# Kernel tuning notes

Hardware: AMD Instinct MI355X
Metric: run time of the kernel (lower is better)

Reference implementation:

```python
import jax, jax.numpy as jnp
import numpy as np

V, P, TY, D, H, L, B, T = 30522, 512, 2, 768, 12, 12, 8, 512
DF = 4 * D


def layer_norm(x, g, b, eps=1e-5):
    m = jnp.mean(x, axis=-1, keepdims=True)
    v = jnp.var(x, axis=-1, keepdims=True)
    return (x - m) * jax.lax.rsqrt(v + eps) * g + b


def new_gelu(x):
    c = np.sqrt(2.0 / np.pi).astype(np.float32)
    return 0.5 * x * (1.0 + jnp.tanh(c * (x + 0.044715 * x * x * x)))


def setup_inputs() -> dict:
    key = jax.random.key(0)
    ks = jax.random.split(key, 10)
    s = 0.02
    n = lambda k, shape: (jax.random.normal(k, shape, jnp.float32) * s)
    return dict(
        input_ids=jax.random.randint(ks[0], (B, T), 0, V),
        token_type_ids=jax.random.randint(ks[1], (B, T), 0, TY),
        attention_mask=jnp.ones((B, T), jnp.float32),
        word_emb=n(ks[2], (V, D)),
        pos_emb=n(ks[3], (P, D)),
        type_emb=n(ks[4], (TY, D)),
        emb_ln_g=jnp.ones((D,), jnp.float32), emb_ln_b=jnp.zeros((D,), jnp.float32),
        ln1_g=jnp.ones((L, D), jnp.float32), ln1_b=jnp.zeros((L, D), jnp.float32),
        wqkv=n(ks[5], (L, D, 3 * D)), bqkv=jnp.zeros((L, 3 * D), jnp.float32),
        wproj=n(ks[6], (L, D, D)) / np.sqrt(2 * L).astype(np.float32),
        bproj=jnp.zeros((L, D), jnp.float32),
        ln2_g=jnp.ones((L, D), jnp.float32), ln2_b=jnp.zeros((L, D), jnp.float32),
        wfc=n(ks[7], (L, D, DF)), bfc=jnp.zeros((L, DF), jnp.float32),
        wfc2=n(ks[8], (L, DF, D)) / np.sqrt(2 * L).astype(np.float32),
        bfc2=jnp.zeros((L, D), jnp.float32),
    )


def reference(input_ids, token_type_ids, attention_mask, word_emb, pos_emb, type_emb,
              emb_ln_g, emb_ln_b, ln1_g, ln1_b, wqkv, bqkv, wproj, bproj,
              ln2_g, ln2_b, wfc, bfc, wfc2, bfc2):
    Bx, Tx = input_ids.shape
    hd = D // H
    scale = np.float32(1.0 / np.sqrt(hd))
    # embeddings: word + position + token-type, then LayerNorm (dropout = 0)
    x = word_emb[input_ids] + pos_emb[:Tx][None, :, :] + type_emb[token_type_ids]
    x = layer_norm(x, emb_ln_g, emb_ln_b)
    # additive mask bias, broadcast over heads and query positions: [B,1,1,T]
    mask_bias = (1.0 - attention_mask)[:, None, None, :] * (-10000.0)

    def block(x, p):
        l1g, l1b, wq, bq, wp, bp, l2g, l2b, wf, bf, w2, b2 = p
        h = layer_norm(x, l1g, l1b)
        qkv = h @ wq + bq                                   # [B,T,3D]
        q, k, v = jnp.split(qkv, 3, axis=-1)
        q = q.reshape(Bx, Tx, H, hd).transpose(0, 2, 1, 3)  # [B,H,T,hd]
        k = k.reshape(Bx, Tx, H, hd).transpose(0, 2, 1, 3)
        v = v.reshape(Bx, Tx, H, hd).transpose(0, 2, 1, 3)
        att = jnp.einsum('bhqd,bhkd->bhqk', q, k) * scale + mask_bias
        att = jax.nn.softmax(att, axis=-1)
        y = jnp.einsum('bhqk,bhkd->bhqd', att, v)
        y = y.transpose(0, 2, 1, 3).reshape(Bx, Tx, D)
        x = x + (y @ wp + bp)                               # attn residual
        h2 = layer_norm(x, l2g, l2b)
        h2 = new_gelu(h2 @ wf + bf) @ w2 + b2               # GELU MLP
        return x + h2, None

    x, _ = jax.lax.scan(block, x, (ln1_g, ln1_b, wqkv, bqkv, wproj, bproj,
                                   ln2_g, ln2_b, wfc, bfc, wfc2, bfc2))
    # baseline MLM head: weight tied to word embeddings, no bias
    logits = x @ word_emb.T                                 # [B,T,V]
    return logits
```

## Files before the change

### kernel.cpp

```cpp
#include <hip/hip_runtime.h>
#include <hip/hip_bf16.h>

typedef unsigned short u16;
typedef __attribute__((ext_vector_type(4))) float f32x4;
typedef __attribute__((ext_vector_type(8))) __bf16 bf16x8;

#define DEV static __device__ __forceinline__

DEV float b2f(u16 v) { return __uint_as_float(((unsigned)v) << 16); }

DEV u16 f2b(float f) {
  unsigned u = __float_as_uint(f);
  return (u16)((u + 0x7fffu + ((u >> 16) & 1u)) >> 16);
}

DEV unsigned pk2(float a, float b) {
  return (unsigned)f2b(a) | ((unsigned)f2b(b) << 16);
}

DEV void gload16(const void* g, void* l) {
  __builtin_amdgcn_global_load_lds(
      (__attribute__((address_space(1))) void*)g,
      (__attribute__((address_space(3))) void*)l, 16, 0, 0);
}

DEV float wave_sum(float v) {
  #pragma unroll
  for (int o = 32; o; o >>= 1) v += __shfl_xor(v, o, 64);
  return v;
}

__global__ __launch_bounds__(256)
void embed_ln_k(const int* __restrict__ ids, const int* __restrict__ tts,
                const float* __restrict__ we, const float* __restrict__ pe,
                const float* __restrict__ te, const float* __restrict__ g,
                const float* __restrict__ bb, float* __restrict__ x) {
  const int t = blockIdx.x;
  const int pos = t & 511;
  const int tid = threadIdx.x, lane = tid & 63, w = tid >> 6;
  const int id = ids[t], tt = tts[t];
  __shared__ float red[8];
  float e[3];
  #pragma unroll
  for (int k = 0; k < 3; k++) {
    int d = tid + k * 256;
    e[k] = we[(size_t)id * 768 + d] + pe[(size_t)pos * 768 + d] + te[(size_t)tt * 768 + d];
  }
  float s = wave_sum(e[0] + e[1] + e[2]);
  if (lane == 0) red[w] = s;
  __syncthreads();
  const float mean = (red[0] + red[1] + red[2] + red[3]) * (1.f / 768.f);
  float v2 = 0.f;
  #pragma unroll
  for (int k = 0; k < 3; k++) { float d = e[k] - mean; v2 += d * d; }
  v2 = wave_sum(v2);
  if (lane == 0) red[4 + w] = v2;
  __syncthreads();
  const float var = (red[4] + red[5] + red[6] + red[7]) * (1.f / 768.f);
  const float rstd = rsqrtf(var + 1e-5f);
  #pragma unroll
  for (int k = 0; k < 3; k++) {
    int d = tid + k * 256;
    x[(size_t)t * 768 + d] = (e[k] - mean) * rstd * g[d] + bb[d];
  }
}

__global__ __launch_bounds__(256)
void ln_k(const float* __restrict__ xin, const float* __restrict__ g,
          const float* __restrict__ bb, u16* __restrict__ out) {
  const int lane = threadIdx.x & 63, w = threadIdx.x >> 6;
  const int t = blockIdx.x * 4 + w;
  const float4* x4 = (const float4*)(xin + (size_t)t * 768);
  float4 e[3];
  #pragma unroll
  for (int k = 0; k < 3; k++) e[k] = x4[k * 64 + lane];
  float s = 0.f;
  #pragma unroll
  for (int k = 0; k < 3; k++) s += e[k].x + e[k].y + e[k].z + e[k].w;
  s = wave_sum(s);
  const float mean = s * (1.f / 768.f);
  float v2 = 0.f;
  #pragma unroll
  for (int k = 0; k < 3; k++) {
    float a = e[k].x - mean, b = e[k].y - mean, c = e[k].z - mean, d = e[k].w - mean;
    v2 += a * a + b * b + c * c + d * d;
  }
  v2 = wave_sum(v2);
  const float rstd = rsqrtf(v2 * (1.f / 768.f) + 1e-5f);
  uint2* o2 = (uint2*)(out + (size_t)t * 768);
  #pragma unroll
  for (int k = 0; k < 3; k++) {
    float4 gv = ((const float4*)g)[k * 64 + lane];
    float4 bv = ((const float4*)bb)[k * 64 + lane];
    uint2 o;
    o.x = pk2((e[k].x - mean) * rstd * gv.x + bv.x, (e[k].y - mean) * rstd * gv.y + bv.y);
    o.y = pk2((e[k].z - mean) * rstd * gv.z + bv.z, (e[k].w - mean) * rstd * gv.w + bv.w);
    o2[k * 64 + lane] = o;
  }
}

__global__ __launch_bounds__(256)
void cast_k(const float* __restrict__ xin, u16* __restrict__ out) {
  const int i = blockIdx.x * 256 + threadIdx.x;
  float4 v = ((const float4*)xin)[i];
  uint2 o;
  o.x = pk2(v.x, v.y);
  o.y = pk2(v.z, v.w);
  ((uint2*)out)[i] = o;
}

__global__ __launch_bounds__(256)
void wecast_k(const float* __restrict__ we, u16* __restrict__ out) {
  const int i = blockIdx.x * 256 + threadIdx.x;
  const int row = i / 96, c8 = i % 96;
  uint2 o0 = make_uint2(0u, 0u), o1 = make_uint2(0u, 0u);
  if (row < 30522) {
    const float* src = we + (size_t)row * 768 + c8 * 8;
    float4 a = ((const float4*)src)[0];
    float4 b = ((const float4*)src)[1];
    o0.x = pk2(a.x, a.y); o0.y = pk2(a.z, a.w);
    o1.x = pk2(b.x, b.y); o1.y = pk2(b.z, b.w);
  }
  uint2* dst = (uint2*)(out + (size_t)i * 8);
  dst[0] = o0;
  dst[1] = o1;
}

DEV void tconv_tile(const float* __restrict__ W, u16* __restrict__ Wt,
                    int K, int N, int n0, int k0, int tid, u16 (*t)[65]) {
  const int kl = tid >> 4, nl4 = (tid & 15) * 4;
  #pragma unroll
  for (int i = 0; i < 4; i++) {
    float4 v = *(const float4*)(W + (size_t)(k0 + kl + i * 16) * N + n0 + nl4);
    t[nl4 + 0][kl + i * 16] = f2b(v.x);
    t[nl4 + 1][kl + i * 16] = f2b(v.y);
    t[nl4 + 2][kl + i * 16] = f2b(v.z);
    t[nl4 + 3][kl + i * 16] = f2b(v.w);
  }
  __syncthreads();
  const int nl = tid >> 2, kc = (tid & 3) * 16;
  unsigned wd[8];
  #pragma unroll
  for (int j = 0; j < 8; j++)
    wd[j] = (unsigned)t[nl][kc + 2 * j] | ((unsigned)t[nl][kc + 2 * j + 1] << 16);
  int4* dst = (int4*)(Wt + (size_t)(n0 + nl) * K + k0 + kc);
  dst[0] = make_int4((int)wd[0], (int)wd[1], (int)wd[2], (int)wd[3]);
  dst[1] = make_int4((int)wd[4], (int)wd[5], (int)wd[6], (int)wd[7]);
}

__global__ __launch_bounds__(256)
void tconv_k(const float* __restrict__ W, u16* __restrict__ Wt, int K, int N) {
  __shared__ u16 t[64][65];
  tconv_tile(W, Wt, K, N, blockIdx.x * 64, blockIdx.y * 64, threadIdx.x, t);
}

__global__ __launch_bounds__(256)
void tconv_all_k(const float* __restrict__ wqkv, const float* __restrict__ wprj,
                 const float* __restrict__ wfc, const float* __restrict__ wfc2,
                 u16* __restrict__ wall) {
  __shared__ u16 ts[64][65];
  const int tile = blockIdx.x;
  const int l = tile / 1728, t = tile % 1728;
  u16* base = wall + (size_t)l * 7077888;
  const float* W; u16* Wt; int K, N, loc;
  if (t < 432)       { W = wqkv + (size_t)l * 768 * 2304; Wt = base;           K = 768;  N = 2304; loc = t; }
  else if (t < 576)  { W = wprj + (size_t)l * 768 * 768;  Wt = base + 1769472; K = 768;  N = 768;  loc = t - 432; }
  else if (t < 1152) { W = wfc  + (size_t)l * 768 * 3072; Wt = base + 2359296; K = 768;  N = 3072; loc = t - 576; }
  else               { W = wfc2 + (size_t)l * 3072 * 768; Wt = base + 4718592; K = 3072; N = 768;  loc = t - 1152; }
  const int nbl = N >> 6;
  tconv_tile(W, Wt, K, N, (loc % nbl) * 64, (loc / nbl) * 64, threadIdx.x, ts);
}

template <int EPI>
__global__ __launch_bounds__(256)
void gemm_k(const u16* __restrict__ A, const u16* __restrict__ B,
            const float* __restrict__ bias, const float* __restrict__ resid,
            void* __restrict__ Cptr, int Ndim, int Kdim, int Nblk) {
  __shared__ __align__(16) u16 As[128 * 64];
  __shared__ __align__(16) u16 Bs[128 * 64];
  const int tid = threadIdx.x, lane = tid & 63, w = tid >> 6;
  const int wr = w >> 1, wc = w & 1, fr = lane & 15, fq = lane >> 4;

  const int nwg = gridDim.x, chunk = nwg >> 3;
  const int tile = (blockIdx.x & 7) * chunk + (blockIdx.x >> 3);
  const int nb = tile % Nblk, mb = tile / Nblk;
  const int n0 = nb * 128, m0 = mb * 128;

  f32x4 acc[4][4] = {};
  const int rl = lane >> 3;
  const int sl = ((lane & 7) ^ rl) * 8;

  for (int k0 = 0; k0 < Kdim; k0 += 64) {
    #pragma unroll
    for (int i = 0; i < 4; i++) {
      const int row = i * 32 + w * 8 + rl;
      gload16(A + (size_t)(m0 + row) * Kdim + k0 + sl, As + (i * 32 + w * 8) * 64);
      gload16(B + (size_t)(n0 + row) * Kdim + k0 + sl, Bs + (i * 32 + w * 8) * 64);
    }
    __syncthreads();
    #pragma unroll
    for (int kh = 0; kh < 2; kh++) {
      const int ks = ((kh * 4 + fq) ^ (fr & 7)) * 8;
      bf16x8 af[4], bfv[4];
      #pragma unroll
      for (int m = 0; m < 4; m++)
        af[m] = *(const bf16x8*)(&As[(wr * 64 + m * 16 + fr) * 64 + ks]);
      #pragma unroll
      for (int n = 0; n < 4; n++)
        bfv[n] = *(const bf16x8*)(&Bs[(wc * 64 + n * 16 + fr) * 64 + ks]);
      #pragma unroll
      for (int m = 0; m < 4; m++)
        #pragma unroll
        for (int n = 0; n < 4; n++)
          acc[m][n] = __builtin_amdgcn_mfma_f32_16x16x32_bf16(af[m], bfv[n], acc[m][n], 0, 0, 0);
    }
    __syncthreads();
  }

  #pragma unroll
  for (int m = 0; m < 4; m++) {
    const int row = m0 + wr * 64 + m * 16 + fq * 4;
    #pragma unroll
    for (int n = 0; n < 4; n++) {
      const int col = n0 + wc * 64 + n * 16 + fr;
      const float bv = (bias != nullptr) ? bias[col] : 0.f;
      #pragma unroll
      for (int r = 0; r < 4; r++) {
        float v = acc[m][n][r] + bv;
        const size_t idx = (size_t)(row + r) * Ndim + col;
        if (EPI == 0) {
          ((u16*)Cptr)[idx] = f2b(v);
        } else if (EPI == 1) {
          float t = v;
          float gl = 0.5f * t * (1.f + tanhf(0.7978845608f * (t + 0.044715f * t * t * t)));
          ((u16*)Cptr)[idx] = f2b(gl);
        } else if (EPI == 2) {
          ((float*)Cptr)[idx] = resid[idx] + v;
        }
      }
    }
  }
}

template <int EPI>
__global__ __launch_bounds__(256)
void gemm64_k(const u16* __restrict__ A, const u16* __restrict__ B,
              const float* __restrict__ bias, const float* __restrict__ resid,
              void* __restrict__ Cptr, int Ndim, int Kdim, int Nblk) {
  __shared__ __align__(16) u16 As[64 * 64];
  __shared__ __align__(16) u16 Bs[64 * 64];
  const int tid = threadIdx.x, lane = tid & 63, w = tid >> 6;
  const int wr = w >> 1, wc = w & 1, fr = lane & 15, fq = lane >> 4;

  const int nwg = gridDim.x, chunk = nwg >> 3;
  const int tile = (blockIdx.x & 7) * chunk + (blockIdx.x >> 3);
  const int nb = tile % Nblk, mb = tile / Nblk;
  const int n0 = nb * 64, m0 = mb * 64;

  f32x4 acc[2][2] = {};
  const int rl = lane >> 3;
  const int sl = ((lane & 7) ^ rl) * 8;

  for (int k0 = 0; k0 < Kdim; k0 += 64) {
    #pragma unroll
    for (int i = 0; i < 2; i++) {
      const int row = i * 32 + w * 8 + rl;
      gload16(A + (size_t)(m0 + row) * Kdim + k0 + sl, As + (i * 32 + w * 8) * 64);
      gload16(B + (size_t)(n0 + row) * Kdim + k0 + sl, Bs + (i * 32 + w * 8) * 64);
    }
    __syncthreads();
    #pragma unroll
    for (int kh = 0; kh < 2; kh++) {
      const int ks = ((kh * 4 + fq) ^ (fr & 7)) * 8;
      bf16x8 af[2], bfv[2];
      #pragma unroll
      for (int m = 0; m < 2; m++)
        af[m] = *(const bf16x8*)(&As[(wr * 32 + m * 16 + fr) * 64 + ks]);
      #pragma unroll
      for (int n = 0; n < 2; n++)
        bfv[n] = *(const bf16x8*)(&Bs[(wc * 32 + n * 16 + fr) * 64 + ks]);
      #pragma unroll
      for (int m = 0; m < 2; m++)
        #pragma unroll
        for (int n = 0; n < 2; n++)
          acc[m][n] = __builtin_amdgcn_mfma_f32_16x16x32_bf16(af[m], bfv[n], acc[m][n], 0, 0, 0);
    }
    __syncthreads();
  }

  #pragma unroll
  for (int m = 0; m < 2; m++) {
    const int row = m0 + wr * 32 + m * 16 + fq * 4;
    #pragma unroll
    for (int n = 0; n < 2; n++) {
      const int col = n0 + wc * 32 + n * 16 + fr;
      const float bv = (bias != nullptr) ? bias[col] : 0.f;
      #pragma unroll
      for (int r = 0; r < 4; r++) {
        float v = acc[m][n][r] + bv;
        const size_t idx = (size_t)(row + r) * Ndim + col;
        if (EPI == 0) {
          ((u16*)Cptr)[idx] = f2b(v);
        } else if (EPI == 1) {
          float t = v;
          float gl = 0.5f * t * (1.f + tanhf(0.7978845608f * (t + 0.044715f * t * t * t)));
          ((u16*)Cptr)[idx] = f2b(gl);
        } else if (EPI == 2) {
          ((float*)Cptr)[idx] = resid[idx] + v;
        }
      }
    }
  }
}

__global__ __launch_bounds__(256)
void gemm256_k(const u16* __restrict__ A, const u16* __restrict__ B,
               float* __restrict__ Cptr, int Ndim, int Kdim, int Nblk) {
  __shared__ __align__(16) u16 As[256 * 64];
  __shared__ __align__(16) u16 Bs[128 * 64];
  const int tid = threadIdx.x, lane = tid & 63, w = tid >> 6;
  const int fr = lane & 15, fq = lane >> 4;

  const int nwg = gridDim.x, chunk = nwg >> 3;
  const int tile = (blockIdx.x & 7) * chunk + (blockIdx.x >> 3);
  const int nb = tile % Nblk, mb = tile / Nblk;
  const int n0 = nb * 128, m0 = mb * 256;

  f32x4 acc[4][8] = {};
  const int rl = lane >> 3;
  const int sl = ((lane & 7) ^ rl) * 8;

  for (int k0 = 0; k0 < Kdim; k0 += 64) {
    #pragma unroll
    for (int i = 0; i < 8; i++) {
      const int row = i * 32 + w * 8 + rl;
      gload16(A + (size_t)(m0 + row) * Kdim + k0 + sl, As + (i * 32 + w * 8) * 64);
    }
    #pragma unroll
    for (int i = 0; i < 4; i++) {
      const int row = i * 32 + w * 8 + rl;
      gload16(B + (size_t)(n0 + row) * Kdim + k0 + sl, Bs + (i * 32 + w * 8) * 64);
    }
    __syncthreads();
    #pragma unroll
    for (int kh = 0; kh < 2; kh++) {
      const int ks = ((kh * 4 + fq) ^ (fr & 7)) * 8;
      bf16x8 af[4], bfv[8];
      #pragma unroll
      for (int m = 0; m < 4; m++)
        af[m] = *(const bf16x8*)(&As[(w * 64 + m * 16 + fr) * 64 + ks]);
      #pragma unroll
      for (int n = 0; n < 8; n++)
        bfv[n] = *(const bf16x8*)(&Bs[(n * 16 + fr) * 64 + ks]);
      #pragma unroll
      for (int m = 0; m < 4; m++)
        #pragma unroll
        for (int n = 0; n < 8; n++)
          acc[m][n] = __builtin_amdgcn_mfma_f32_16x16x32_bf16(af[m], bfv[n], acc[m][n], 0, 0, 0);
    }
    __syncthreads();
  }

  #pragma unroll
  for (int m = 0; m < 4; m++) {
    const int row = m0 + w * 64 + m * 16 + fq * 4;
    #pragma unroll
    for (int n = 0; n < 8; n++) {
      const int col = n0 + n * 16 + fr;
      if (col >= Ndim) continue;
      #pragma unroll
      for (int r = 0; r < 4; r++)
        Cptr[(size_t)(row + r) * Ndim + col] = acc[m][n][r];
    }
  }
}

__global__ __launch_bounds__(256)
void attn_mfma_k(const u16* __restrict__ qkv, const float* __restrict__ amask,
                 u16* __restrict__ y) {
  __shared__ __align__(16) u16 Ks[2][64 * 64];
  __shared__ __align__(16) u16 Vt[2][64 * 64];
  __shared__ __align__(16) u16 Ps[4][16 * 64];
  __shared__ float bias_lds[512];
  const int tid = threadIdx.x, lane = tid & 63, w = tid >> 6;
  const int bh = blockIdx.y, b = bh / 12, hh = bh % 12;
  const int q0 = blockIdx.x * 64;
  const u16* qb = qkv + (size_t)(b * 512) * 2304 + hh * 64;
  const u16* kb = qb + 768;
  const u16* vb = qb + 1536;
  const int fr = lane & 15, fq = lane >> 4;

  bias_lds[tid] = (1.0f - amask[b * 512 + tid]) * -10000.0f;
  bias_lds[tid + 256] = (1.0f - amask[b * 512 + tid + 256]) * -10000.0f;

  bf16x8 af[2];
  {
    const u16* qrow = qb + (size_t)(q0 + w * 16 + fr) * 2304;
    af[0] = *(const bf16x8*)(qrow + fq * 8);
    af[1] = *(const bf16x8*)(qrow + 32 + fq * 8);
  }

  auto stageK = [&](int kt, int nb) {
    const int r0 = lane >> 3, dc = lane & 7, s = dc ^ r0;
    #pragma unroll
    for (int p = 0; p < 2; p++) {
      const int i = w * 2 + p;
      gload16(kb + (size_t)(kt * 64 + i * 8 + r0) * 2304 + s * 8,
              (void*)&Ks[nb][i * 512]);
    }
  };
  auto stageV = [&](int kt, int nb) {
    #pragma unroll
    for (int p = 0; p < 2; p++) {
      const int dc = w * 2 + p;
      int4 vd = *(const int4*)(vb + (size_t)(kt * 64 + lane) * 2304 + dc * 8);
      union { int4 v; u16 e[8]; } u; u.v = vd;
      #pragma unroll
      for (int ii = 0; ii < 8; ii++)
        Vt[nb][(dc * 8 + ii) * 64 + (lane ^ (ii << 3))] = u.e[ii];
    }
  };

  f32x4 O[4];
  #pragma unroll
  for (int nd = 0; nd < 4; nd++) O[nd] = f32x4{0.f, 0.f, 0.f, 0.f};
  float run_m = -3.0e38f, run_l = 0.f;

  stageK(0, 0); stageV(0, 0);
  __syncthreads();
  int cur = 0;

  for (int kt = 0; kt < 8; kt++) {
    if (kt < 7) { stageK(kt + 1, cur ^ 1); stageV(kt + 1, cur ^ 1); }

    f32x4 sacc[4];
    #pragma unroll
    for (int n = 0; n < 4; n++) sacc[n] = f32x4{0.f, 0.f, 0.f, 0.f};
    __builtin_amdgcn_s_setprio(1);
    #pragma unroll
    for (int n = 0; n < 4; n++)
      #pragma unroll
      for (int kh = 0; kh < 2; kh++) {
        bf16x8 kf = *(const bf16x8*)(&Ks[cur][(n * 16 + fr) * 64 + ((kh * 4 + fq) ^ (fr & 7)) * 8]);
        sacc[n] = __builtin_amdgcn_mfma_f32_16x16x32_bf16(kf, af[kh], sacc[n], 0, 0, 0);
      }
    __builtin_amdgcn_s_setprio(0);

    float s[4][4];
    float vm = -3.0e38f;
    #pragma unroll
    for (int n = 0; n < 4; n++) {
      float4 b4 = *(const float4*)(&bias_lds[kt * 64 + n * 16 + fq * 4]);
      s[n][0] = sacc[n][0] * 0.125f + b4.x;
      s[n][1] = sacc[n][1] * 0.125f + b4.y;
      s[n][2] = sacc[n][2] * 0.125f + b4.z;
      s[n][3] = sacc[n][3] * 0.125f + b4.w;
      vm = fmaxf(vm, fmaxf(fmaxf(s[n][0], s[n][1]), fmaxf(s[n][2], s[n][3])));
    }
    vm = fmaxf(vm, __shfl_xor(vm, 16, 64));
    vm = fmaxf(vm, __shfl_xor(vm, 32, 64));
    const float nm = fmaxf(run_m, vm);
    const float al = __expf(run_m - nm);
    run_m = nm;
    float p[4][4], ts = 0.f;
    #pragma unroll
    for (int n = 0; n < 4; n++)
      #pragma unroll
      for (int r = 0; r < 4; r++) { p[n][r] = __expf(s[n][r] - nm); ts += p[n][r]; }
    ts += __shfl_xor(ts, 16, 64);
    ts += __shfl_xor(ts, 32, 64);
    run_l = run_l * al + ts;
    #pragma unroll
    for (int nd = 0; nd < 4; nd++) O[nd] *= al;

    #pragma unroll
    for (int n = 0; n < 4; n++) {
      uint2 dw;
      dw.x = pk2(p[n][0], p[n][1]);
      dw.y = pk2(p[n][2], p[n][3]);
      const int slot = (2 * n + (fq >> 1)) ^ (fr & 7);
      *(uint2*)((char*)&Ps[w][0] + fr * 128 + slot * 16 + (fq & 1) * 8) = dw;
    }
    asm volatile("s_waitcnt lgkmcnt(0)" ::: "memory");
    __builtin_amdgcn_sched_barrier(0);

    bf16x8 pb[2];
    #pragma unroll
    for (int kh = 0; kh < 2; kh++)
      pb[kh] = *(const bf16x8*)((char*)&Ps[w][0] + fr * 128 + (((kh * 4 + fq) ^ (fr & 7)) * 16));
    __builtin_amdgcn_s_setprio(1);
    #pragma unroll
    for (int nd = 0; nd < 4; nd++) {
      bf16x8 vf0 = *(const bf16x8*)(&Vt[cur][(nd * 16 + fr) * 64 + ((0 + fq) ^ (fr & 7)) * 8]);
      bf16x8 vf1 = *(const bf16x8*)(&Vt[cur][(nd * 16 + fr) * 64 + ((4 + fq) ^ (fr & 7)) * 8]);
      O[nd] = __builtin_amdgcn_mfma_f32_16x16x32_bf16(vf0, pb[0], O[nd], 0, 0, 0);
      O[nd] = __builtin_amdgcn_mfma_f32_16x16x32_bf16(vf1, pb[1], O[nd], 0, 0, 0);
    }
    __builtin_amdgcn_s_setprio(0);
    __syncthreads();
    cur ^= 1;
  }

  const float inv = 1.0f / run_l;
  u16* yrow = y + (size_t)(b * 512 + q0 + w * 16 + fr) * 768 + hh * 64;
  #pragma unroll
  for (int nd = 0; nd < 4; nd++) {
    uint2 o;
    o.x = pk2(O[nd][0] * inv, O[nd][1] * inv);
    o.y = pk2(O[nd][2] * inv, O[nd][3] * inv);
    *(uint2*)(yrow + nd * 16 + fq * 4) = o;
  }
}

extern "C" void kernel_launch(void* const* d_in, const int* in_sizes, int n_in,
                              void* d_out, int out_size, void* d_ws, size_t ws_size,
                              hipStream_t stream) {
  (void)in_sizes; (void)n_in; (void)out_size;
  const int*   ids  = (const int*)d_in[0];
  const int*   tts  = (const int*)d_in[1];
  const float* am   = (const float*)d_in[2];
  const float* we   = (const float*)d_in[3];
  const float* pe   = (const float*)d_in[4];
  const float* te   = (const float*)d_in[5];
  const float* eg   = (const float*)d_in[6];
  const float* eb   = (const float*)d_in[7];
  const float* l1g  = (const float*)d_in[8];
  const float* l1b  = (const float*)d_in[9];
  const float* wqkv = (const float*)d_in[10];
  const float* bqkv = (const float*)d_in[11];
  const float* wprj = (const float*)d_in[12];
  const float* bprj = (const float*)d_in[13];
  const float* l2g  = (const float*)d_in[14];
  const float* l2b  = (const float*)d_in[15];
  const float* wfc  = (const float*)d_in[16];
  const float* bfc  = (const float*)d_in[17];
  const float* wfc2 = (const float*)d_in[18];
  const float* bfc2 = (const float*)d_in[19];

  char* ws = (char*)d_ws;
  float* x   = (float*)ws;
  u16*  h    = (u16*)(ws + 12582912);
  u16*  qkv  = (u16*)(ws + 18874368);
  u16*  y    = (u16*)(ws + 37748736);
  u16*  fc   = (u16*)(ws + 18874368);
  u16*  we_b = (u16*)(ws + 44040192);
  u16*  wall = (u16*)(ws + 91029504);
  const bool upfront = ws_size >= 260898816ull;
  u16* wqkv_f = (u16*)(ws + 91029504);
  u16* wprj_f = wqkv_f + 1769472;
  u16* wfc_f  = wqkv_f + 2359296;
  u16* wfc2_f = wqkv_f + 4718592;

  wecast_k<<<11472, 256, 0, stream>>>(we, we_b);
  embed_ln_k<<<4096, 256, 0, stream>>>(ids, tts, we, pe, te, eg, eb, x);
  if (upfront)
    tconv_all_k<<<20736, 256, 0, stream>>>(wqkv, wprj, wfc, wfc2, wall);

  for (int l = 0; l < 12; l++) {
    u16 *wq_b, *wp_b, *wf_b, *w2_b;
    if (upfront) {
      u16* base = wall + (size_t)l * 7077888;
      wq_b = base; wp_b = base + 1769472; wf_b = base + 2359296; w2_b = base + 4718592;
    } else {
      tconv_k<<<dim3(36, 12), 256, 0, stream>>>(wqkv + (size_t)l * 768 * 2304, wqkv_f, 768, 2304);
      tconv_k<<<dim3(12, 12), 256, 0, stream>>>(wprj + (size_t)l * 768 * 768,  wprj_f, 768, 768);
      tconv_k<<<dim3(48, 12), 256, 0, stream>>>(wfc  + (size_t)l * 768 * 3072, wfc_f,  768, 3072);
      tconv_k<<<dim3(12, 48), 256, 0, stream>>>(wfc2 + (size_t)l * 3072 * 768, wfc2_f, 3072, 768);
      wq_b = wqkv_f; wp_b = wprj_f; wf_b = wfc_f; w2_b = wfc2_f;
    }

    ln_k<<<1024, 256, 0, stream>>>(x, l1g + l * 768, l1b + l * 768, h);
    gemm_k<0><<<576, 256, 0, stream>>>(
        h, wq_b, bqkv + l * 2304, nullptr, qkv, 2304, 768, 18);
    attn_mfma_k<<<dim3(8, 96), 256, 0, stream>>>(qkv, am, y);
    gemm64_k<2><<<768, 256, 0, stream>>>(
        y, wp_b, bprj + l * 768, x, x, 768, 768, 12);
    ln_k<<<1024, 256, 0, stream>>>(x, l2g + l * 768, l2b + l * 768, h);
    gemm_k<1><<<768, 256, 0, stream>>>(
        h, wf_b, bfc + l * 3072, nullptr, fc, 3072, 768, 24);
    gemm64_k<2><<<768, 256, 0, stream>>>(
        fc, w2_b, bfc2 + l * 768, x, x, 768, 3072, 12);
  }

  cast_k<<<3072, 256, 0, stream>>>(x, h);
  gemm256_k<<<3824, 256, 0, stream>>>(
      h, we_b, (float*)d_out, 30522, 768, 239);
}
```

Baseline: 2.425 ms.

## Double-buffer LDS tiles in the 256x128 logits GEMM

Reworks the gemm256 kernel (the MLM-head logits GEMM) to use two LDS buffers with a K-step of 32 instead of one buffer with a K-step of 64. The next tile's global-to-LDS load is issued before the MFMAs on the current tile run. This removes one of the two barriers per step and overlaps memory latency with compute. In exchange it runs twice as many loop iterations, with a narrower swizzle and fewer MFMAs between barriers, and the total LDS footprint stays the same.

```diff
diff --git a/kernel.cpp b/kernel.cpp
--- a/kernel.cpp
+++ b/kernel.cpp
@@ -316,8 +316,8 @@
 __global__ __launch_bounds__(256)
 void gemm256_k(const u16* __restrict__ A, const u16* __restrict__ B,
                float* __restrict__ Cptr, int Ndim, int Kdim, int Nblk) {
-  __shared__ __align__(16) u16 As[256 * 64];
-  __shared__ __align__(16) u16 Bs[128 * 64];
+  __shared__ __align__(16) u16 As[2][256 * 32];
+  __shared__ __align__(16) u16 Bs[2][128 * 32];
   const int tid = threadIdx.x, lane = tid & 63, w = tid >> 6;
   const int fr = lane & 15, fq = lane >> 4;
 
@@ -327,39 +327,48 @@
   const int n0 = nb * 128, m0 = mb * 256;
 
   f32x4 acc[4][8] = {};
-  const int rl = lane >> 3;
-  const int sl = ((lane & 7) ^ rl) * 8;
-
-  for (int k0 = 0; k0 < Kdim; k0 += 64) {
-    #pragma unroll
-    for (int i = 0; i < 8; i++) {
-      const int row = i * 32 + w * 8 + rl;
-      gload16(A + (size_t)(m0 + row) * Kdim + k0 + sl, As + (i * 32 + w * 8) * 64);
-    }
-    #pragma unroll
-    for (int i = 0; i < 4; i++) {
-      const int row = i * 32 + w * 8 + rl;
-      gload16(B + (size_t)(n0 + row) * Kdim + k0 + sl, Bs + (i * 32 + w * 8) * 64);
-    }
+  const int r0l = lane >> 2;
+  const int sl = ((lane & 3) ^ (r0l & 3)) * 8;
+
+  #define STAGE256(k0, buf)                                                     \
+    {                                                                           \
+      _Pragma("unroll")                                                         \
+      for (int i = 0; i < 4; i++) {                                             \
+        const int st = i * 4 + w;                                               \
+        gload16(A + (size_t)(m0 + st * 16 + r0l) * Kdim + (k0) + sl,            \
+                &As[buf][st * 512]);                                            \
+      }                                                                         \
+      _Pragma("unroll")                                                         \
+      for (int i = 0; i < 2; i++) {                                             \
+        const int st = i * 4 + w;                                               \
+        gload16(B + (size_t)(n0 + st * 16 + r0l) * Kdim + (k0) + sl,            \
+                &Bs[buf][st * 512]);                                            \
+      }                                                                         \
+    }
+
+  STAGE256(0, 0);
+  __syncthreads();
+  int buf = 0;
+
+  for (int k0 = 0; k0 < Kdim; k0 += 32) {
+    if (k0 + 32 < Kdim) STAGE256(k0 + 32, buf ^ 1);
+    const int ks = (fq ^ (fr & 3)) * 8;
+    bf16x8 af[4], bfv[8];
+    #pragma unroll
+    for (int m = 0; m < 4; m++)
+      af[m] = *(const bf16x8*)(&As[buf][(w * 64 + m * 16 + fr) * 32 + ks]);
+    #pragma unroll
+    for (int n = 0; n < 8; n++)
+      bfv[n] = *(const bf16x8*)(&Bs[buf][(n * 16 + fr) * 32 + ks]);
+    #pragma unroll
+    for (int m = 0; m < 4; m++)
+      #pragma unroll
+      for (int n = 0; n < 8; n++)
+        acc[m][n] = __builtin_amdgcn_mfma_f32_16x16x32_bf16(af[m], bfv[n], acc[m][n], 0, 0, 0);
     __syncthreads();
-    #pragma unroll
-    for (int kh = 0; kh < 2; kh++) {
-      const int ks = ((kh * 4 + fq) ^ (fr & 7)) * 8;
-      bf16x8 af[4], bfv[8];
-      #pragma unroll
-      for (int m = 0; m < 4; m++)
-        af[m] = *(const bf16x8*)(&As[(w * 64 + m * 16 + fr) * 64 + ks]);
-      #pragma unroll
-      for (int n = 0; n < 8; n++)
-        bfv[n] = *(const bf16x8*)(&Bs[(n * 16 + fr) * 64 + ks]);
-      #pragma unroll
-      for (int m = 0; m < 4; m++)
-        #pragma unroll
-        for (int n = 0; n < 8; n++)
-          acc[m][n] = __builtin_amdgcn_mfma_f32_16x16x32_bf16(af[m], bfv[n], acc[m][n], 0, 0, 0);
-    }
-    __syncthreads();
-  }
+    buf ^= 1;
+  }
+  #undef STAGE256
 
   #pragma unroll
   for (int m = 0; m < 4; m++) {
```

New measurement: 2.298 ms. -5.2%, faster.
